# Kernel tuning notes

Measured on AMD Instinct MI355X. Metric: run time of the kernel, lower is better.

The kernel has to match this reference:

```python
import jax, jax.numpy as jnp
import numpy as np

B, N, C, H, DEPTH = 64, 256, 384, 8, 6
HD = C // H  # 48
SCALE = HD ** -0.5
LN_EPS = 1e-5


def setup_inputs() -> dict:
    key = jax.random.key(0)
    ks = jax.random.split(key, 12)
    g = lambda k, shape, s=0.05: jax.random.normal(k, shape, jnp.float32) * s
    return {
        "x": jax.random.normal(ks[0], (B, N, 2), jnp.float32),
        "mask": jnp.zeros((B, N), jnp.float32),  # additive padding mask (0 = keep)
        "emb_w1": g(ks[1], (C, 2), 0.5),
        "emb_b1": jnp.zeros((C,), jnp.float32),
        "emb_w2": g(ks[2], (C, C)),
        "emb_b2": jnp.zeros((C,), jnp.float32),
        "qkv_w": g(ks[3], (DEPTH, 3 * C, C)),
        "proj_w": g(ks[4], (DEPTH, C, C)),
        "proj_b": jnp.zeros((DEPTH, C), jnp.float32),
        "mlp_w1": g(ks[5], (DEPTH, C, C)),
        "mlp_b1": jnp.zeros((DEPTH, C), jnp.float32),
        "mlp_w2": g(ks[6], (DEPTH, C, C)),
        "mlp_b2": jnp.zeros((DEPTH, C), jnp.float32),
        "ln1_s": jnp.ones((DEPTH, C), jnp.float32),
        "ln1_b": jnp.zeros((DEPTH, C), jnp.float32),
        "ln2_s": jnp.ones((DEPTH, C), jnp.float32),
        "ln2_b": jnp.zeros((DEPTH, C), jnp.float32),
    }


def _layernorm(x, s, b):
    mu = jnp.mean(x, axis=-1, keepdims=True)
    var = jnp.mean((x - mu) ** 2, axis=-1, keepdims=True)
    return (x - mu) * jax.lax.rsqrt(var + LN_EPS) * s + b


def _rope(t):
    # t: (B, H, N, HD); interleaved rotary, matching the torch module
    hd = t.shape[-1]
    inv_freq = 1.0 / (10000.0 ** (jnp.arange(0, hd, 2, dtype=jnp.float32) / hd))
    pos = jnp.arange(t.shape[2], dtype=jnp.float32)
    f = pos[:, None] * inv_freq[None, :]            # (N, HD/2)
    cos, sin = jnp.cos(f), jnp.sin(f)
    xu, xe = t[..., 0::2], t[..., 1::2]
    ru = xu * cos - xe * sin
    re = xu * sin + xe * cos
    return jnp.stack([ru, re], axis=-1).reshape(t.shape)


def reference(x, mask, emb_w1, emb_b1, emb_w2, emb_b2, qkv_w, proj_w, proj_b,
              mlp_w1, mlp_b1, mlp_w2, mlp_b2, ln1_s, ln1_b, ln2_s, ln2_b):
    # BallEmbedding: Linear -> ReLU -> Linear
    h = jax.nn.relu(x @ emb_w1.T + emb_b1) @ emb_w2.T + emb_b2  # (B, N, C)
    for i in range(DEPTH):
        # pre-norm rotary attention
        y = _layernorm(h, ln1_s[i], ln1_b[i])
        qkv = (y @ qkv_w[i].T).reshape(B, N, 3, H, HD).transpose(2, 0, 3, 1, 4)
        q, k, v = qkv[0], qkv[1], qkv[2]                      # (B, H, N, HD)
        q = _rope(q) * SCALE
        k = _rope(k)
        attn = jnp.einsum('bhqd,bhkd->bhqk', q, k)
        attn = attn + mask[:, None, None, :] + mask[:, None, :, None]
        attn = jax.nn.softmax(attn, axis=-1)
        o = jnp.einsum('bhqk,bhkd->bhqd', attn, v)
        o = o.transpose(0, 2, 1, 3).reshape(B, N, C)
        h = h + (o @ proj_w[i].T + proj_b[i])
        # pre-norm MLP (hidden = dim, ReLU)
        y = _layernorm(h, ln2_s[i], ln2_b[i])
        m = jax.nn.relu(y @ mlp_w1[i].T + mlp_b1[i]) @ mlp_w2[i].T + mlp_b2[i]
        h = h + m
    return h
```

## Files before the change

kernel.cpp:

```cpp
#include <hip/hip_runtime.h>
#include <hip/hip_bf16.h>
#include <math.h>

#define BATCH 64
#define SEQ   256
#define CH    384
#define NHEAD 8
#define HD    48
#define DEPTH 6
#define NTOK  (BATCH*SEQ)
#define C3    (3*CH)
#define LN_EPS 1e-5f
#define ATT_SCALE 0.14433756729740643f

typedef __attribute__((ext_vector_type(8)))  short bf16x8;
typedef __attribute__((ext_vector_type(4)))  float f32x4;
typedef __attribute__((ext_vector_type(16))) float f32x16;

__device__ __forceinline__ ushort f2bf(float f) {
    __hip_bfloat16 h = __float2bfloat16(f);
    return *(ushort*)&h;
}
__device__ __forceinline__ float bfu2f(ushort u) {
    uint t = ((uint)u) << 16;
    union { uint u; float f; } c; c.u = t; return c.f;
}
__device__ __forceinline__ uint pk2(float a, float b) {
    return (uint)f2bf(a) | ((uint)f2bf(b) << 16);
}

#define AS1(p) ((const __attribute__((address_space(1))) void*)(p))
#define AS3(p) ((__attribute__((address_space(3))) void*)(uintptr_t)(p))
#define WAITVMC(N) asm volatile("s_waitcnt vmcnt(" #N ")" ::: "memory")
#define TAILSYNC() do { \
    asm volatile("s_waitcnt lgkmcnt(0)" ::: "memory"); \
    __builtin_amdgcn_sched_barrier(0); \
    __builtin_amdgcn_s_barrier(); } while (0)

__global__ void zero_kernel(float4* __restrict__ p) {
    p[blockIdx.x*256 + threadIdx.x] = float4{0.f,0.f,0.f,0.f};
}

__global__ void f2bf4_kernel(const float* __restrict__ in, ushort* __restrict__ out) {
    int i = (blockIdx.x*256 + threadIdx.x)*4;
    float4 v = *(const float4*)(in + i);
    ushort4 o;
    o.x = f2bf(v.x); o.y = f2bf(v.y); o.z = f2bf(v.z); o.w = f2bf(v.w);
    *(ushort4*)(out + i) = o;
}

__global__ void rope_table_kernel(float2* __restrict__ tbl) {
    int pos = threadIdx.x;
    for (int j = 0; j < 24; ++j) {
        float freq = exp2f(-(float)j * (13.287712379549449f / 24.0f));
        float ang = (float)pos * freq;
        float s, c;
        sincosf(ang, &s, &c);
        tbl[pos*24 + j] = make_float2(c, s);
    }
}

__global__ void embed1_kernel(const float* __restrict__ x, const float* __restrict__ w1,
                              const float* __restrict__ b1, ushort* __restrict__ out) {
    int idx = blockIdx.x*256 + threadIdx.x;
    int m = idx / CH, c = idx - m*CH;
    float v = x[m*2]*w1[c*2] + x[m*2+1]*w1[c*2+1] + b1[c];
    out[idx] = f2bf(fmaxf(v, 0.f));
}

__global__ __launch_bounds__(256) void prep_kernel(
        const float* __restrict__ Wsrc, const float* __restrict__ gam,
        const float* __restrict__ bet, const float* __restrict__ bias,
        int npl, ushort* __restrict__ Wdst, float2* __restrict__ uvout) {
    int rr   = blockIdx.x*4 + (threadIdx.x >> 6);
    int lane = threadIdx.x & 63;
    int layer = rr / npl;
    const float* wp = Wsrc + (size_t)rr*CH;
    const float* gp = gam + layer*CH;
    const float* bp = bet + layer*CH;
    float u = 0.f, vv = 0.f;
    if (lane < 48) {
        int c0 = lane*8;
        float w8[8];
        *(float4*)&w8[0] = *(const float4*)(wp + c0);
        *(float4*)&w8[4] = *(const float4*)(wp + c0 + 4);
        union { ushort us[8]; bf16x8 v; } o;
        #pragma unroll
        for (int j = 0; j < 8; ++j) {
            float wg = w8[j] * gp[c0+j];
            u  += wg;
            vv += bp[c0+j] * w8[j];
            o.us[j] = f2bf(wg);
        }
        *(bf16x8*)(Wdst + (size_t)rr*CH + c0) = o.v;
    }
    #pragma unroll
    for (int o = 1; o < 64; o <<= 1) { u += __shfl_xor(u, o); vv += __shfl_xor(vv, o); }
    if (lane == 0) {
        if (bias) vv += bias[rr];
        uvout[rr] = make_float2(u, vv);
    }
}

template<bool LNAFF, bool RELU, bool RESID, bool QKV>
__global__ __launch_bounds__(256) void gemm_kernel(
        const ushort* __restrict__ A,
        const ushort* __restrict__ W,
        const float*  __restrict__ bias,
        const float2* __restrict__ uv,
        const float2* __restrict__ sbr,
        const float*  __restrict__ resid,
        float*  __restrict__ hout,
        ushort* __restrict__ bout,
        int ldo, int nx,
        float2* __restrict__ sbw,
        ushort* __restrict__ vtbuf,
        const float2* __restrict__ tbl) {
    __shared__ __align__(16) ushort As[2][8192];
    __shared__ __align__(16) ushort Bs[2][8192];
    const int tid  = threadIdx.x;
    const int lane = tid & 63;
    const int w    = tid >> 6;
    const int l15  = lane & 15;
    const int g    = lane >> 4;
    const int wr   = (w >> 1) * 64;
    const int wc   = (w & 1) * 64;
    const int lin  = blockIdx.x;
    const int swz  = (lin & 7)*((int)gridDim.x >> 3) + (lin >> 3);
    const int m0   = (swz / nx) * 128;
    const int n0   = (swz % nx) * 128;

    const int srow = lane >> 3;
    const int scol = ((lane & 7) ^ srow) * 8;
    auto stage = [&](int pb, int t) {
        int k0 = t*64;
        #pragma unroll
        for (int c = 0; c < 8; ++c) {
            int chunk = w + c*4;
            if (chunk < 16) {
                const ushort* gp = A + (size_t)(m0 + chunk*8 + srow)*CH + k0 + scol;
                __builtin_amdgcn_global_load_lds(AS1(gp), AS3(&As[pb][chunk*512]), 16, 0, 0);
            } else {
                const ushort* gp = W + (size_t)(n0 + (chunk-16)*8 + srow)*CH + k0 + scol;
                __builtin_amdgcn_global_load_lds(AS1(gp), AS3(&Bs[pb][(chunk-16)*512]), 16, 0, 0);
            }
        }
    };

    f32x4 acc[4][4] = {};
    const int xm = (l15 & 7) << 4;

    stage(0, 0);
    for (int t = 0; t < 6; ++t) {
        if (t + 1 < 6) stage((t+1)&1, t+1);
        if (t < 5) { WAITVMC(8); } else { WAITVMC(0); }
        __builtin_amdgcn_s_barrier();
        const int pb = t & 1;
        #pragma unroll
        for (int kk = 0; kk < 2; ++kk) {
            bf16x8 a[4], b[4];
            #pragma unroll
            for (int i = 0; i < 4; ++i)
                a[i] = *(const bf16x8*)((const char*)As[pb]
                        + (wr + i*16 + l15)*128 + ((kk*64 + 16*g) ^ xm));
            #pragma unroll
            for (int j = 0; j < 4; ++j)
                b[j] = *(const bf16x8*)((const char*)Bs[pb]
                        + (wc + j*16 + l15)*128 + ((kk*64 + 16*g) ^ xm));
            #pragma unroll
            for (int i = 0; i < 4; ++i)
                #pragma unroll
                for (int j = 0; j < 4; ++j)
                    acc[i][j] = __builtin_amdgcn_mfma_f32_16x16x32_bf16(a[i], b[j], acc[i][j], 0, 0, 0);
        }
        TAILSYNC();
    }

    const int cbase = n0 + wc + l15;
    const int rbase = m0 + wr + g*4;
    if (LNAFF) {
        float2 uvv[4];
        #pragma unroll
        for (int j = 0; j < 4; ++j) uvv[j] = uv[cbase + j*16];
        const int region = QKV ? (n0 / 384) : 0;
        int hj[4], dj[4], jp[4];
        if (QKV) {
            #pragma unroll
            for (int j = 0; j < 4; ++j) {
                int nn = cbase + j*16 - region*384;
                if (region == 2) { hj[j] = nn / HD; dj[j] = nn - hj[j]*HD; }
                else             { jp[j] = (nn % HD) >> 1; }
            }
        }
        #pragma unroll
        for (int i = 0; i < 4; ++i) {
            float muv[4], invv[4];
            #pragma unroll
            for (int r = 0; r < 4; ++r) {
                float2 s2 = sbr[rbase + i*16 + r];
                float mu = s2.x * (1.0f/CH);
                float var = s2.y * (1.0f/CH) - mu*mu;
                muv[r] = mu; invv[r] = rsqrtf(var + LN_EPS);
            }
            if (QKV && region == 2) {
                int bb   = rbase >> 8;
                int seq0 = (rbase + i*16) & 255;
                #pragma unroll
                for (int j = 0; j < 4; ++j) {
                    float vr[4];
                    #pragma unroll
                    for (int r = 0; r < 4; ++r)
                        vr[r] = invv[r]*(acc[i][j][r] - muv[r]*uvv[j].x) + uvv[j].y;
                    uint2 val;
                    val.x = pk2(vr[0], vr[1]);
                    val.y = pk2(vr[2], vr[3]);
                    *(uint2*)(vtbuf + (((size_t)bb*NHEAD + hj[j])*64 + dj[j])*SEQ + seq0) = val;
                }
            } else {
                #pragma unroll
                for (int r = 0; r < 4; ++r) {
                    int m = rbase + i*16 + r;
                    int pos = m & 255;
                    #pragma unroll
                    for (int j = 0; j < 4; ++j) {
                        float v = invv[r]*(acc[i][j][r] - muv[r]*uvv[j].x) + uvv[j].y;
                        if (QKV) {
                            float vx = __shfl_xor(v, 1);
                            float2 cs = tbl[pos*24 + jp[j]];
                            v = (l15 & 1) ? (vx*cs.y + v*cs.x) : (v*cs.x - vx*cs.y);
                            if (region == 0) v *= ATT_SCALE;
                        }
                        if (RELU) v = fmaxf(v, 0.f);
                        bout[(size_t)m*ldo + cbase + j*16] = f2bf(v);
                    }
                }
            }
        }
    } else {
        float bj[4];
        #pragma unroll
        for (int j = 0; j < 4; ++j) bj[j] = bias[cbase + j*16];
        #pragma unroll
        for (int i = 0; i < 4; ++i)
            #pragma unroll
            for (int r = 0; r < 4; ++r) {
                int m = rbase + i*16 + r;
                #pragma unroll
                for (int j = 0; j < 4; ++j) {
                    int n = cbase + j*16;
                    float v = acc[i][j][r] + bj[j];
                    if (RESID) v += resid[(size_t)m*CH + n];
                    acc[i][j][r] = v;
                    hout[(size_t)m*CH + n] = v;
                    bout[(size_t)m*CH + n] = f2bf(v);
                }
            }
        if (sbw) {
            #pragma unroll
            for (int i = 0; i < 4; ++i)
                #pragma unroll
                for (int r = 0; r < 4; ++r) {
                    float s = 0.f, q = 0.f;
                    #pragma unroll
                    for (int j = 0; j < 4; ++j) {
                        float v = acc[i][j][r];
                        s += v; q += v*v;
                    }
                    #pragma unroll
                    for (int off = 1; off < 16; off <<= 1) {
                        s += __shfl_xor(s, off);
                        q += __shfl_xor(q, off);
                    }
                    if (l15 == 0) {
                        int m = rbase + i*16 + r;
                        atomicAdd(&sbw[m].x, s);
                        atomicAdd(&sbw[m].y, q);
                    }
                }
        }
    }
}

__global__ __launch_bounds__(512) void attn_kernel(
        const ushort* __restrict__ qkv, const ushort* __restrict__ vtbuf,
        const float* __restrict__ mask, ushort* __restrict__ obuf) {
    __shared__ __align__(16) ushort Kf[8*3*64*8];
    __shared__ __align__(16) ushort Vf[2*16*64*8];
    __shared__ float Ms[SEQ];

    const int bid = blockIdx.x;
    const int b   = bid >> 3;
    const int hh  = bid & 7;
    const int tid = threadIdx.x;
    const int lane = tid & 63;
    const int hi   = (lane >> 5);
    const int q5   = lane & 31;
    const int twv  = tid >> 6;
    const ushort* base = qkv + (size_t)b*SEQ*C3;

    {
        int row = twv*32 + q5;
        const ushort* kp = base + (size_t)row*C3 + CH + hh*HD + hi*8;
        #pragma unroll
        for (int s = 0; s < 3; ++s)
            __builtin_amdgcn_global_load_lds(AS1(kp + s*16), AS3(&Kf[(twv*3+s)*512]), 16, 0, 0);
    }
    {
        const ushort* vt = vtbuf + (size_t)(b*NHEAD + hh)*64*SEQ;
        #pragma unroll
        for (int p = 0; p < 4; ++p) {
            int dt = p >> 1;
            int sp = twv*2 + (p & 1);
            int dd = dt*32 + q5;
            const ushort* vp = vt + (size_t)dd*SEQ + sp*16 + hi*8;
            __builtin_amdgcn_global_load_lds(AS1(vp), AS3(&Vf[(dt*16+sp)*512]), 16, 0, 0);
        }
    }
    if (tid < SEQ) Ms[tid] = mask[b*SEQ + tid];

    const int qrow = twv*32 + q5;
    bf16x8 qf[3];
    {
        const ushort* qp = base + (size_t)qrow*C3 + hh*HD + hi*8;
        #pragma unroll
        for (int s = 0; s < 3; ++s) qf[s] = *(const bf16x8*)(qp + s*16);
    }
    __syncthreads();

    f32x16 st[8] = {};
    #pragma unroll
    for (int t = 0; t < 8; ++t)
        #pragma unroll
        for (int s = 0; s < 3; ++s) {
            bf16x8 af = *(const bf16x8*)&Kf[((t*3 + s)*64 + lane)*8];
            st[t] = __builtin_amdgcn_mfma_f32_32x32x16_bf16(af, qf[s], st[t], 0, 0, 0);
        }

    float mx = -1e30f;
    #pragma unroll
    for (int t = 0; t < 8; ++t)
        #pragma unroll
        for (int r = 0; r < 16; ++r) {
            int kt = t*32 + (r & 3) + 8*(r >> 2) + 4*hi;
            float s = st[t][r] + Ms[kt];
            st[t][r] = s;
            mx = fmaxf(mx, s);
        }
    mx = fmaxf(mx, __shfl_xor(mx, 32));
    float sum = 0.f;
    #pragma unroll
    for (int t = 0; t < 8; ++t)
        #pragma unroll
        for (int r = 0; r < 16; ++r) {
            float p = __expf(st[t][r] - mx);
            st[t][r] = p;
            sum += p;
        }
    sum += __shfl_xor(sum, 32);

    f32x16 oacc[2] = {};
    #pragma unroll
    for (int t = 0; t < 8; ++t) {
        uint w[4][2];
        #pragma unroll
        for (int g = 0; g < 4; ++g) {
            w[g][0] = pk2(st[t][g*4+0], st[t][g*4+1]);
            w[g][1] = pk2(st[t][g*4+2], st[t][g*4+3]);
        }
        #pragma unroll
        for (int o = 0; o < 2; ++o) {
            uint x0 = __shfl_xor(hi ? w[2*o][0] : w[2*o+1][0], 32);
            uint x1 = __shfl_xor(hi ? w[2*o][1] : w[2*o+1][1], 32);
            union { uint w[4]; bf16x8 v; } pf;
            if (hi == 0) { pf.w[0] = w[2*o][0]; pf.w[1] = w[2*o][1]; pf.w[2] = x0; pf.w[3] = x1; }
            else         { pf.w[0] = x0; pf.w[1] = x1; pf.w[2] = w[2*o+1][0]; pf.w[3] = w[2*o+1][1]; }
            int sp = t*2 + o;
            #pragma unroll
            for (int dt = 0; dt < 2; ++dt) {
                bf16x8 vf = *(const bf16x8*)&Vf[((dt*16 + sp)*64 + lane)*8];
                oacc[dt] = __builtin_amdgcn_mfma_f32_32x32x16_bf16(vf, pf.v, oacc[dt], 0, 0, 0);
            }
        }
    }

    float inv = 1.f / sum;
    ushort* op = obuf + ((size_t)(b*SEQ + qrow))*CH + hh*HD;
    #pragma unroll
    for (int dt = 0; dt < 2; ++dt)
        #pragma unroll
        for (int rg = 0; rg < 4; ++rg) {
            int d0 = dt*32 + rg*8 + hi*4;
            if (d0 < HD) {
                uint2 val;
                val.x = pk2(oacc[dt][rg*4+0]*inv, oacc[dt][rg*4+1]*inv);
                val.y = pk2(oacc[dt][rg*4+2]*inv, oacc[dt][rg*4+3]*inv);
                *(uint2*)(op + d0) = val;
            }
        }
}

extern "C" void kernel_launch(void* const* d_in, const int* in_sizes, int n_in,
                              void* d_out, int out_size, void* d_ws, size_t ws_size,
                              hipStream_t stream) {
    const float* x      = (const float*)d_in[0];
    const float* mask   = (const float*)d_in[1];
    const float* emb_w1 = (const float*)d_in[2];
    const float* emb_b1 = (const float*)d_in[3];
    const float* emb_w2 = (const float*)d_in[4];
    const float* emb_b2 = (const float*)d_in[5];
    const float* qkv_w  = (const float*)d_in[6];
    const float* proj_w = (const float*)d_in[7];
    const float* proj_b = (const float*)d_in[8];
    const float* mlp_w1 = (const float*)d_in[9];
    const float* mlp_b1 = (const float*)d_in[10];
    const float* mlp_w2 = (const float*)d_in[11];
    const float* mlp_b2 = (const float*)d_in[12];
    const float* ln1_s  = (const float*)d_in[13];
    const float* ln1_b  = (const float*)d_in[14];
    const float* ln2_s  = (const float*)d_in[15];
    const float* ln2_b  = (const float*)d_in[16];

    const size_t S1 = (size_t)NTOK*CH;
    float*  h     = (float*)d_ws;
    ushort* hbf   = (ushort*)(h + S1);
    ushort* qkvbf = hbf + S1;
    ushort* ybf   = qkvbf + 3*S1;
    ushort* t2bf  = ybf  + S1;
    ushort* obf   = t2bf + S1;
    ushort* vtbuf = obf  + S1;
    ushort* wb_emb2 = vtbuf + (size_t)BATCH*NHEAD*64*SEQ;
    ushort* wb_proj = wb_emb2 + 147456;
    ushort* wb_m2   = wb_proj + 884736;
    ushort* wqkvp   = wb_m2   + 884736;
    ushort* wm1p    = wqkvp   + 2654208;
    float2* uv_qkv  = (float2*)(wm1p + 884736);
    float2* uv_m1   = uv_qkv + 6912;
    float2* sb      = uv_m1  + 2304;
    float*  tbl     = (float*)(sb + 12*NTOK);
    const float2* tblc = (const float2*)tbl;

    zero_kernel<<<384, 256, 0, stream>>>((float4*)sb);
    rope_table_kernel<<<1, 256, 0, stream>>>((float2*)tbl);
    f2bf4_kernel<<<144, 256, 0, stream>>>(emb_w2, wb_emb2);
    f2bf4_kernel<<<864, 256, 0, stream>>>(proj_w, wb_proj);
    f2bf4_kernel<<<864, 256, 0, stream>>>(mlp_w2, wb_m2);
    prep_kernel<<<1728, 256, 0, stream>>>(qkv_w,  ln1_s, ln1_b, nullptr, C3, wqkvp, uv_qkv);
    prep_kernel<<<576,  256, 0, stream>>>(mlp_w1, ln2_s, ln2_b, mlp_b1,  CH, wm1p,  uv_m1);

    embed1_kernel<<<(NTOK*CH)/256, 256, 0, stream>>>(x, emb_w1, emb_b1, ybf);
    gemm_kernel<false,false,false,false><<<384, 256, 0, stream>>>(ybf, wb_emb2, emb_b2,
            nullptr, nullptr, nullptr, h, hbf, CH, 3, sb, nullptr, nullptr);

    for (int i = 0; i < DEPTH; ++i) {
        gemm_kernel<true,false,false,true><<<1152, 256, 0, stream>>>(hbf,
                wqkvp + (size_t)i*C3*CH, nullptr, uv_qkv + i*C3, sb + (size_t)(2*i)*NTOK,
                nullptr, nullptr, qkvbf, C3, 9, nullptr, vtbuf, tblc);
        attn_kernel<<<BATCH*NHEAD, 512, 0, stream>>>(qkvbf, vtbuf, mask, obf);
        gemm_kernel<false,false,true,false><<<384, 256, 0, stream>>>(obf,
                wb_proj + (size_t)i*CH*CH, proj_b + i*CH, nullptr, nullptr,
                h, h, hbf, CH, 3, sb + (size_t)(2*i+1)*NTOK, nullptr, nullptr);
        gemm_kernel<true,true,false,false><<<384, 256, 0, stream>>>(hbf,
                wm1p + (size_t)i*CH*CH, nullptr, uv_m1 + i*CH, sb + (size_t)(2*i+1)*NTOK,
                nullptr, nullptr, t2bf, CH, 3, nullptr, nullptr, nullptr);
        gemm_kernel<false,false,true,false><<<384, 256, 0, stream>>>(t2bf,
                wb_m2 + (size_t)i*CH*CH, mlp_b2 + i*CH, nullptr, nullptr,
                h, h, hbf, CH, 3, (i < DEPTH-1) ? (sb + (size_t)(2*i+2)*NTOK) : nullptr,
                nullptr, nullptr);
    }
    hipMemcpyAsync(d_out, h, S1*sizeof(float), hipMemcpyDeviceToDevice, stream);
}
```

Measured before the change: 851.4 us.

## Halve GEMM M-tile to 64 rows and merge setup kernels

The GEMM block tile shrinks from 128x128 to 64x128, so each wave covers 32 rows instead of 64 and the grids double (384→768, 1152→2304). This is meant to fill more of the CUs and raise occupancy with less LDS and fewer accumulator registers per block. The cost is lower data reuse per block and more redundant weight-tile loads. The zero, rope-table and three weight-conversion kernels are also folded into two launches to cut launch overhead.

```diff
diff --git a/kernel.cpp b/kernel.cpp
--- a/kernel.cpp
+++ b/kernel.cpp
@@ -37,27 +37,35 @@
     __builtin_amdgcn_sched_barrier(0); \
     __builtin_amdgcn_s_barrier(); } while (0)
 
-__global__ void zero_kernel(float4* __restrict__ p) {
-    p[blockIdx.x*256 + threadIdx.x] = float4{0.f,0.f,0.f,0.f};
-}
-
-__global__ void f2bf4_kernel(const float* __restrict__ in, ushort* __restrict__ out) {
-    int i = (blockIdx.x*256 + threadIdx.x)*4;
-    float4 v = *(const float4*)(in + i);
+__global__ void init_kernel(float4* __restrict__ sb, float2* __restrict__ tbl) {
+    int bid = blockIdx.x;
+    if (bid < 384) {
+        sb[bid*256 + threadIdx.x] = float4{0.f,0.f,0.f,0.f};
+    } else {
+        int pos = threadIdx.x;
+        for (int j = 0; j < 24; ++j) {
+            float freq = exp2f(-(float)j * (13.287712379549449f / 24.0f));
+            float ang = (float)pos * freq;
+            float s, c;
+            sincosf(ang, &s, &c);
+            tbl[pos*24 + j] = make_float2(c, s);
+        }
+    }
+}
+
+__global__ void f2bf3_kernel(const float* __restrict__ s0, const float* __restrict__ s1,
+                             const float* __restrict__ s2, ushort* __restrict__ dst) {
+    int bid = blockIdx.x;
+    const float* src;
+    int loc;
+    if (bid < 144)      { src = s0; loc = bid; }
+    else if (bid < 1008){ src = s1; loc = bid - 144; }
+    else                { src = s2; loc = bid - 1008; }
+    int li = loc*1024 + threadIdx.x*4;
+    float4 v = *(const float4*)(src + li);
     ushort4 o;
     o.x = f2bf(v.x); o.y = f2bf(v.y); o.z = f2bf(v.z); o.w = f2bf(v.w);
-    *(ushort4*)(out + i) = o;
-}
-
-__global__ void rope_table_kernel(float2* __restrict__ tbl) {
-    int pos = threadIdx.x;
-    for (int j = 0; j < 24; ++j) {
-        float freq = exp2f(-(float)j * (13.287712379549449f / 24.0f));
-        float ang = (float)pos * freq;
-        float s, c;
-        sincosf(ang, &s, &c);
-        tbl[pos*24 + j] = make_float2(c, s);
-    }
+    *(ushort4*)(dst + (size_t)bid*1024 + threadIdx.x*4) = o;
 }
 
 __global__ void embed1_kernel(const float* __restrict__ x, const float* __restrict__ w1,
@@ -116,18 +124,18 @@
         float2* __restrict__ sbw,
         ushort* __restrict__ vtbuf,
         const float2* __restrict__ tbl) {
-    __shared__ __align__(16) ushort As[2][8192];
+    __shared__ __align__(16) ushort As[2][4096];
     __shared__ __align__(16) ushort Bs[2][8192];
     const int tid  = threadIdx.x;
     const int lane = tid & 63;
     const int w    = tid >> 6;
     const int l15  = lane & 15;
     const int g    = lane >> 4;
-    const int wr   = (w >> 1) * 64;
+    const int wr   = (w >> 1) * 32;
     const int wc   = (w & 1) * 64;
     const int lin  = blockIdx.x;
     const int swz  = (lin & 7)*((int)gridDim.x >> 3) + (lin >> 3);
-    const int m0   = (swz / nx) * 128;
+    const int m0   = (swz / nx) * 64;
     const int n0   = (swz % nx) * 128;
 
     const int srow = lane >> 3;
@@ -135,32 +143,32 @@
     auto stage = [&](int pb, int t) {
         int k0 = t*64;
         #pragma unroll
-        for (int c = 0; c < 8; ++c) {
+        for (int c = 0; c < 6; ++c) {
             int chunk = w + c*4;
-            if (chunk < 16) {
+            if (chunk < 8) {
                 const ushort* gp = A + (size_t)(m0 + chunk*8 + srow)*CH + k0 + scol;
                 __builtin_amdgcn_global_load_lds(AS1(gp), AS3(&As[pb][chunk*512]), 16, 0, 0);
             } else {
-                const ushort* gp = W + (size_t)(n0 + (chunk-16)*8 + srow)*CH + k0 + scol;
-                __builtin_amdgcn_global_load_lds(AS1(gp), AS3(&Bs[pb][(chunk-16)*512]), 16, 0, 0);
+                const ushort* gp = W + (size_t)(n0 + (chunk-8)*8 + srow)*CH + k0 + scol;
+                __builtin_amdgcn_global_load_lds(AS1(gp), AS3(&Bs[pb][(chunk-8)*512]), 16, 0, 0);
             }
         }
     };
 
-    f32x4 acc[4][4] = {};
+    f32x4 acc[2][4] = {};
     const int xm = (l15 & 7) << 4;
 
     stage(0, 0);
     for (int t = 0; t < 6; ++t) {
         if (t + 1 < 6) stage((t+1)&1, t+1);
-        if (t < 5) { WAITVMC(8); } else { WAITVMC(0); }
+        if (t < 5) { WAITVMC(6); } else { WAITVMC(0); }
         __builtin_amdgcn_s_barrier();
         const int pb = t & 1;
         #pragma unroll
         for (int kk = 0; kk < 2; ++kk) {
-            bf16x8 a[4], b[4];
-            #pragma unroll
-            for (int i = 0; i < 4; ++i)
+            bf16x8 a[2], b[4];
+            #pragma unroll
+            for (int i = 0; i < 2; ++i)
                 a[i] = *(const bf16x8*)((const char*)As[pb]
                         + (wr + i*16 + l15)*128 + ((kk*64 + 16*g) ^ xm));
             #pragma unroll
@@ -168,7 +176,7 @@
                 b[j] = *(const bf16x8*)((const char*)Bs[pb]
                         + (wc + j*16 + l15)*128 + ((kk*64 + 16*g) ^ xm));
             #pragma unroll
-            for (int i = 0; i < 4; ++i)
+            for (int i = 0; i < 2; ++i)
                 #pragma unroll
                 for (int j = 0; j < 4; ++j)
                     acc[i][j] = __builtin_amdgcn_mfma_f32_16x16x32_bf16(a[i], b[j], acc[i][j], 0, 0, 0);
@@ -193,7 +201,7 @@
             }
         }
         #pragma unroll
-        for (int i = 0; i < 4; ++i) {
+        for (int i = 0; i < 2; ++i) {
             float muv[4], invv[4];
             #pragma unroll
             for (int r = 0; r < 4; ++r) {
@@ -241,7 +249,7 @@
         #pragma unroll
         for (int j = 0; j < 4; ++j) bj[j] = bias[cbase + j*16];
         #pragma unroll
-        for (int i = 0; i < 4; ++i)
+        for (int i = 0; i < 2; ++i)
             #pragma unroll
             for (int r = 0; r < 4; ++r) {
                 int m = rbase + i*16 + r;
@@ -257,7 +265,7 @@
             }
         if (sbw) {
             #pragma unroll
-            for (int i = 0; i < 4; ++i)
+            for (int i = 0; i < 2; ++i)
                 #pragma unroll
                 for (int r = 0; r < 4; ++r) {
                     float s = 0.f, q = 0.f;
@@ -439,30 +447,27 @@
     float*  tbl     = (float*)(sb + 12*NTOK);
     const float2* tblc = (const float2*)tbl;
 
-    zero_kernel<<<384, 256, 0, stream>>>((float4*)sb);
-    rope_table_kernel<<<1, 256, 0, stream>>>((float2*)tbl);
-    f2bf4_kernel<<<144, 256, 0, stream>>>(emb_w2, wb_emb2);
-    f2bf4_kernel<<<864, 256, 0, stream>>>(proj_w, wb_proj);
-    f2bf4_kernel<<<864, 256, 0, stream>>>(mlp_w2, wb_m2);
+    init_kernel<<<385, 256, 0, stream>>>((float4*)sb, (float2*)tbl);
+    f2bf3_kernel<<<1872, 256, 0, stream>>>(emb_w2, proj_w, mlp_w2, wb_emb2);
     prep_kernel<<<1728, 256, 0, stream>>>(qkv_w,  ln1_s, ln1_b, nullptr, C3, wqkvp, uv_qkv);
     prep_kernel<<<576,  256, 0, stream>>>(mlp_w1, ln2_s, ln2_b, mlp_b1,  CH, wm1p,  uv_m1);
 
     embed1_kernel<<<(NTOK*CH)/256, 256, 0, stream>>>(x, emb_w1, emb_b1, ybf);
-    gemm_kernel<false,false,false,false><<<384, 256, 0, stream>>>(ybf, wb_emb2, emb_b2,
+    gemm_kernel<false,false,false,false><<<768, 256, 0, stream>>>(ybf, wb_emb2, emb_b2,
             nullptr, nullptr, nullptr, h, hbf, CH, 3, sb, nullptr, nullptr);
 
     for (int i = 0; i < DEPTH; ++i) {
-        gemm_kernel<true,false,false,true><<<1152, 256, 0, stream>>>(hbf,
+        gemm_kernel<true,false,false,true><<<2304, 256, 0, stream>>>(hbf,
                 wqkvp + (size_t)i*C3*CH, nullptr, uv_qkv + i*C3, sb + (size_t)(2*i)*NTOK,
                 nullptr, nullptr, qkvbf, C3, 9, nullptr, vtbuf, tblc);
         attn_kernel<<<BATCH*NHEAD, 512, 0, stream>>>(qkvbf, vtbuf, mask, obf);
-        gemm_kernel<false,false,true,false><<<384, 256, 0, stream>>>(obf,
+        gemm_kernel<false,false,true,false><<<768, 256, 0, stream>>>(obf,
                 wb_proj + (size_t)i*CH*CH, proj_b + i*CH, nullptr, nullptr,
                 h, h, hbf, CH, 3, sb + (size_t)(2*i+1)*NTOK, nullptr, nullptr);
-        gemm_kernel<true,true,false,false><<<384, 256, 0, stream>>>(hbf,
+        gemm_kernel<true,true,false,false><<<768, 256, 0, stream>>>(hbf,
                 wm1p + (size_t)i*CH*CH, nullptr, uv_m1 + i*CH, sb + (size_t)(2*i+1)*NTOK,
                 nullptr, nullptr, t2bf, CH, 3, nullptr, nullptr, nullptr);
-        gemm_kernel<false,false,true,false><<<384, 256, 0, stream>>>(t2bf,
+        gemm_kernel<false,false,true,false><<<768, 256, 0, stream>>>(t2bf,
                 wb_m2 + (size_t)i*CH*CH, mlp_b2 + i*CH, nullptr, nullptr,
                 h, h, hbf, CH, 3, (i < DEPTH-1) ? (sb + (size_t)(2*i+2)*NTOK) : nullptr,
                 nullptr, nullptr);
```

Result: no change. 846.5 us (-0.6%).
